# Kernel tuning notes

Hardware: AMD Instinct MI355X
Metric: run time of the kernel (lower is better)

The kernel has to match this reference:

```python
import jax, jax.numpy as jnp
import numpy as np

B, T, C, H = 8, 1024, 1024, 16
D = C // H  # head size 64
EPS = 1e-5

def layernorm(x, g, b):
    m = jnp.mean(x, axis=-1, keepdims=True)
    v = jnp.var(x, axis=-1, keepdims=True)
    return (x - m) * jax.lax.rsqrt(v + EPS) * g + b

def setup_inputs() -> dict:
    key = jax.random.key(0)
    ks = jax.random.split(key, 12)
    s = 1.0 / np.sqrt(C)
    return {
        "x": jax.random.normal(ks[0], (B, T, C), dtype=jnp.float32),
        "mask": jnp.ones((B, 1, 1, T), dtype=jnp.int32),
        "Wq": jax.random.normal(ks[1], (C, C), dtype=jnp.float32) * s,
        "Wk": jax.random.normal(ks[2], (C, C), dtype=jnp.float32) * s,
        "Wv": jax.random.normal(ks[3], (C, C), dtype=jnp.float32) * s,
        "Wo": jax.random.normal(ks[4], (C, C), dtype=jnp.float32) * s,
        "bo": jnp.zeros((C,), dtype=jnp.float32),
        "ln1_g": jnp.ones((C,), dtype=jnp.float32),
        "ln1_b": jnp.zeros((C,), dtype=jnp.float32),
        "ln3_g": jnp.ones((C,), dtype=jnp.float32),
        "ln3_b": jnp.zeros((C,), dtype=jnp.float32),
        "W1": jax.random.normal(ks[5], (C, 4 * C), dtype=jnp.float32) * s,
        "b1": jnp.zeros((4 * C,), dtype=jnp.float32),
        "W2": jax.random.normal(ks[6], (4 * C, C), dtype=jnp.float32) * (1.0 / np.sqrt(4 * C)),
        "b2": jnp.zeros((C,), dtype=jnp.float32),
    }

def reference(x, mask, Wq, Wk, Wv, Wo, bo, ln1_g, ln1_b, ln3_g, ln3_b, W1, b1, W2, b2):
    # --- self-attention sublayer (pre-LN, residual) ---
    xn = layernorm(x, ln1_g, ln1_b)                      # [B,T,C]
    q = (xn @ Wq).reshape(B, T, H, D)                    # [B,T,H,D]
    k = (xn @ Wk).reshape(B, T, H, D)
    v = (xn @ Wv).reshape(B, T, H, D)
    scores = jnp.einsum('bqhd,bkhd->bhqk', q, k) / np.sqrt(D)  # [B,H,T,T]
    scores = jnp.where(mask == 0, -jnp.inf, scores)      # padding mask [B,1,1,T] broadcasts
    attn = jax.nn.softmax(scores, axis=-1)               # dropout=0.0 -> identity
    o = jnp.einsum('bhqk,bkhd->bqhd', attn, v).reshape(B, T, C)
    x = x + o @ Wo + bo
    # --- feed-forward sublayer (pre-LN, residual) ---
    h = layernorm(x, ln3_g, ln3_b)
    ff = jax.nn.relu(h @ W1 + b1) @ W2 + b2
    return x + ff
```

## Files before the change

### kernel.cpp

```cpp
#include <hip/hip_runtime.h>
#include <stdint.h>

typedef unsigned short u16;
typedef __bf16 bf16x8 __attribute__((ext_vector_type(8)));
typedef float f32x4 __attribute__((ext_vector_type(4)));

#define B_ 8
#define T_ 1024
#define C_ 1024
#define H_ 16
#define D_ 64
#define M_TOT 8192
#define FF_ 4096

__device__ __forceinline__ u16 f2bf(float f) {
  union { float f; unsigned u; } c; c.f = f;
  unsigned u = c.u;
  return (u16)((u + 0x7FFFu + ((u >> 16) & 1u)) >> 16);
}

__device__ __forceinline__ void g2l16(const void* g, void* l) {
  __builtin_amdgcn_global_load_lds((const __attribute__((address_space(1))) void*)g,
                                   (__attribute__((address_space(3))) void*)l, 16, 0, 0);
}

__global__ __launch_bounds__(256) void trans_f32_bf16(const float* __restrict__ in,
                                                      u16* __restrict__ out, int R, int C) {
  __shared__ float t[32][33];
  int c0 = blockIdx.x * 32, r0 = blockIdx.y * 32;
  int tx = threadIdx.x & 31, ty = threadIdx.x >> 5;
#pragma unroll
  for (int i = ty; i < 32; i += 8)
    t[i][tx] = in[(size_t)(r0 + i) * C + c0 + tx];
  __syncthreads();
#pragma unroll
  for (int i = ty; i < 32; i += 8)
    out[(size_t)(c0 + i) * R + r0 + tx] = f2bf(t[tx][i]);
}

__global__ __launch_bounds__(256) void ln_f32_bf16(const float* __restrict__ x,
                                                   const float* __restrict__ g,
                                                   const float* __restrict__ bt,
                                                   u16* __restrict__ out) {
  int row = blockIdx.x, tid = threadIdx.x;
  const float4* xr = (const float4*)(x + (size_t)row * C_);
  float4 a = xr[tid];
  float s = a.x + a.y + a.z + a.w;
  float ss = a.x * a.x + a.y * a.y + a.z * a.z + a.w * a.w;
#pragma unroll
  for (int m = 1; m < 64; m <<= 1) { s += __shfl_xor(s, m); ss += __shfl_xor(ss, m); }
  __shared__ float red[8];
  int wave = tid >> 6, lane = tid & 63;
  if (lane == 0) { red[wave] = s; red[wave + 4] = ss; }
  __syncthreads();
  s = red[0] + red[1] + red[2] + red[3];
  ss = red[4] + red[5] + red[6] + red[7];
  float mean = s * (1.0f / C_);
  float rstd = rsqrtf(ss * (1.0f / C_) - mean * mean + 1e-5f);
  float4 gg = ((const float4*)g)[tid];
  float4 bb = ((const float4*)bt)[tid];
  u16* op = out + (size_t)row * C_ + tid * 4;
  op[0] = f2bf((a.x - mean) * rstd * gg.x + bb.x);
  op[1] = f2bf((a.y - mean) * rstd * gg.y + bb.y);
  op[2] = f2bf((a.z - mean) * rstd * gg.z + bb.z);
  op[3] = f2bf((a.w - mean) * rstd * gg.w + bb.w);
}

template <int EPI>
__global__ __launch_bounds__(256) void gemm_bf16(const u16* __restrict__ A,
                                                 const u16* __restrict__ BT,
                                                 u16* __restrict__ outb, float* __restrict__ outf,
                                                 const float* __restrict__ bias,
                                                 const float* __restrict__ resid,
                                                 int M, int N, int K) {
  __shared__ u16 As[128 * 32];
  __shared__ u16 Bs[128 * 32];
  int tid = threadIdx.x, wave = tid >> 6, lane = tid & 63;
  int m0 = blockIdx.y * 128, n0 = blockIdx.x * 128;
  int wr = wave >> 1, wc = wave & 1;
  int frow = lane & 15, fk = (lane >> 4) * 8;
  f32x4 acc[4][4] = {};
  for (int k0 = 0; k0 < K; k0 += 32) {
    __syncthreads();
#pragma unroll
    for (int i = 0; i < 2; i++) {
      int c = i * 256 + tid;
      const u16* ga = A + (size_t)(m0 + (c >> 2)) * K + k0 + (c & 3) * 8;
      const u16* gb = BT + (size_t)(n0 + (c >> 2)) * K + k0 + (c & 3) * 8;
      g2l16(ga, As + (i * 256 + wave * 64) * 8);
      g2l16(gb, Bs + (i * 256 + wave * 64) * 8);
    }
    asm volatile("s_waitcnt vmcnt(0)" ::: "memory");
    __syncthreads();
    bf16x8 af[4], bfr[4];
#pragma unroll
    for (int m = 0; m < 4; m++) af[m] = *(const bf16x8*)(As + (wr * 64 + m * 16 + frow) * 32 + fk);
#pragma unroll
    for (int n = 0; n < 4; n++) bfr[n] = *(const bf16x8*)(Bs + (wc * 64 + n * 16 + frow) * 32 + fk);
#pragma unroll
    for (int m = 0; m < 4; m++)
#pragma unroll
      for (int n = 0; n < 4; n++)
        acc[m][n] = __builtin_amdgcn_mfma_f32_16x16x32_bf16(af[m], bfr[n], acc[m][n], 0, 0, 0);
  }
#pragma unroll
  for (int m = 0; m < 4; m++)
#pragma unroll
    for (int n = 0; n < 4; n++)
#pragma unroll
      for (int r = 0; r < 4; r++) {
        int row = m0 + wr * 64 + m * 16 + (lane >> 4) * 4 + r;
        int col = n0 + wc * 64 + n * 16 + (lane & 15);
        float v = acc[m][n][r];
        if (EPI == 0) {
          outb[(size_t)row * N + col] = f2bf(v);
        } else if (EPI == 1) {
          v += bias[col];
          v = fmaxf(v, 0.f);
          outb[(size_t)row * N + col] = f2bf(v);
        } else {
          v += bias[col] + resid[(size_t)row * N + col];
          outf[(size_t)row * N + col] = v;
        }
      }
}

__global__ __launch_bounds__(256) void attn_kernel(const u16* __restrict__ q,
                                                   const u16* __restrict__ k,
                                                   const u16* __restrict__ v,
                                                   const int* __restrict__ mask,
                                                   u16* __restrict__ o) {
  int tid = threadIdx.x, wave = tid >> 6, lane = tid & 63;
  int qt = blockIdx.x;
  int bh = blockIdx.y;
  int b = bh >> 4, h = bh & 15;
  const size_t base = ((size_t)b * T_) * C_ + h * D_;

  int qrow = qt * 64 + wave * 16 + (lane & 15);
  int dk = (lane >> 4) * 8;
  bf16x8 qf0 = *(const bf16x8*)(q + base + (size_t)qrow * C_ + dk);
  bf16x8 qf1 = *(const bf16x8*)(q + base + (size_t)qrow * C_ + dk + 32);

  f32x4 oacc[4] = {};
  float mrun[4], lrun[4];
#pragma unroll
  for (int r = 0; r < 4; r++) { mrun[r] = -1e30f; lrun[r] = 0.f; }

  __shared__ u16 vlds[32 * 64];
  __shared__ u16 plds[4][16 * 32];

  for (int kt = 0; kt < T_ / 32; ++kt) {
    __syncthreads();
    {
      int c = tid;
      const u16* gv = v + base + (size_t)(kt * 32 + (c >> 3)) * C_ + (c & 7) * 8;
      g2l16(gv, vlds + wave * 512);
    }
    f32x4 s[2];
#pragma unroll
    for (int c = 0; c < 2; c++) {
      int kcol = kt * 32 + c * 16 + (lane & 15);
      const u16* kp = k + base + (size_t)kcol * C_;
      bf16x8 k0 = *(const bf16x8*)(kp + dk);
      bf16x8 k1 = *(const bf16x8*)(kp + dk + 32);
      f32x4 a = {};
      a = __builtin_amdgcn_mfma_f32_16x16x32_bf16(qf0, k0, a, 0, 0, 0);
      a = __builtin_amdgcn_mfma_f32_16x16x32_bf16(qf1, k1, a, 0, 0, 0);
      int mv = mask[b * T_ + kcol];
#pragma unroll
      for (int r = 0; r < 4; r++) {
        float sv = a[r] * 0.125f;
        a[r] = mv ? sv : -1e30f;
      }
      s[c] = a;
    }
    float tmax[4];
#pragma unroll
    for (int r = 0; r < 4; r++) tmax[r] = fmaxf(s[0][r], s[1][r]);
#pragma unroll
    for (int m = 1; m < 16; m <<= 1)
#pragma unroll
      for (int r = 0; r < 4; r++) tmax[r] = fmaxf(tmax[r], __shfl_xor(tmax[r], m));
    float alpha[4];
#pragma unroll
    for (int r = 0; r < 4; r++) {
      float nm = fmaxf(mrun[r], tmax[r]);
      alpha[r] = __expf(mrun[r] - nm);
      mrun[r] = nm;
    }
    float psum[4] = {0.f, 0.f, 0.f, 0.f};
#pragma unroll
    for (int c = 0; c < 2; c++)
#pragma unroll
      for (int r = 0; r < 4; r++) {
        float p = __expf(s[c][r] - mrun[r]);
        s[c][r] = p;
        psum[r] += p;
      }
#pragma unroll
    for (int m = 1; m < 16; m <<= 1)
#pragma unroll
      for (int r = 0; r < 4; r++) psum[r] += __shfl_xor(psum[r], m);
#pragma unroll
    for (int r = 0; r < 4; r++) lrun[r] = lrun[r] * alpha[r] + psum[r];
#pragma unroll
    for (int n = 0; n < 4; n++)
#pragma unroll
      for (int r = 0; r < 4; r++) oacc[n][r] *= alpha[r];
    u16* pw = plds[wave];
#pragma unroll
    for (int c = 0; c < 2; c++)
#pragma unroll
      for (int r = 0; r < 4; r++)
        pw[((lane >> 4) * 4 + r) * 32 + c * 16 + (lane & 15)] = f2bf(s[c][r]);
    bf16x8 pa = *(const bf16x8*)(pw + (lane & 15) * 32 + (lane >> 4) * 8);

    asm volatile("s_waitcnt vmcnt(0)" ::: "memory");
    __syncthreads();
    const __bf16* vp = (const __bf16*)vlds;
#pragma unroll
    for (int n = 0; n < 4; n++) {
      bf16x8 vb;
#pragma unroll
      for (int j = 0; j < 8; j++) vb[j] = vp[((lane >> 4) * 8 + j) * 64 + n * 16 + (lane & 15)];
      oacc[n] = __builtin_amdgcn_mfma_f32_16x16x32_bf16(pa, vb, oacc[n], 0, 0, 0);
    }
  }
#pragma unroll
  for (int n = 0; n < 4; n++)
#pragma unroll
    for (int r = 0; r < 4; r++) {
      int row = qt * 64 + wave * 16 + (lane >> 4) * 4 + r;
      o[((size_t)b * T_ + row) * C_ + h * D_ + n * 16 + (lane & 15)] =
          f2bf(oacc[n][r] / lrun[r]);
    }
}

extern "C" void kernel_launch(void* const* d_in, const int* in_sizes, int n_in,
                              void* d_out, int out_size, void* d_ws, size_t ws_size,
                              hipStream_t stream) {
  const float* x    = (const float*)d_in[0];
  const int*   mask = (const int*)d_in[1];
  const float* Wq   = (const float*)d_in[2];
  const float* Wk   = (const float*)d_in[3];
  const float* Wv   = (const float*)d_in[4];
  const float* Wo   = (const float*)d_in[5];
  const float* bo   = (const float*)d_in[6];
  const float* ln1g = (const float*)d_in[7];
  const float* ln1b = (const float*)d_in[8];
  const float* ln3g = (const float*)d_in[9];
  const float* ln3b = (const float*)d_in[10];
  const float* W1   = (const float*)d_in[11];
  const float* b1   = (const float*)d_in[12];
  const float* W2   = (const float*)d_in[13];
  const float* b2   = (const float*)d_in[14];
  float* out = (float*)d_out;

  char* ws = (char*)d_ws;
  const size_t MB = 1024 * 1024;
  u16* WqT = (u16*)(ws + 0 * MB);
  u16* WkT = (u16*)(ws + 2 * MB);
  u16* WvT = (u16*)(ws + 4 * MB);
  u16* WoT = (u16*)(ws + 6 * MB);
  u16* W1T = (u16*)(ws + 8 * MB);
  u16* W2T = (u16*)(ws + 16 * MB);
  u16* xn  = (u16*)(ws + 24 * MB);
  u16* qb  = (u16*)(ws + 40 * MB);
  u16* kb  = (u16*)(ws + 56 * MB);
  u16* vb  = (u16*)(ws + 72 * MB);
  u16* ob  = (u16*)(ws + 88 * MB);
  float* x2 = (float*)(ws + 104 * MB);
  u16* hb  = xn;
  u16* ff1 = qb;

  dim3 blk(256);
  trans_f32_bf16<<<dim3(32, 32), blk, 0, stream>>>(Wq, WqT, 1024, 1024);
  trans_f32_bf16<<<dim3(32, 32), blk, 0, stream>>>(Wk, WkT, 1024, 1024);
  trans_f32_bf16<<<dim3(32, 32), blk, 0, stream>>>(Wv, WvT, 1024, 1024);
  trans_f32_bf16<<<dim3(32, 32), blk, 0, stream>>>(Wo, WoT, 1024, 1024);
  trans_f32_bf16<<<dim3(128, 32), blk, 0, stream>>>(W1, W1T, 1024, 4096);
  trans_f32_bf16<<<dim3(32, 128), blk, 0, stream>>>(W2, W2T, 4096, 1024);
  ln_f32_bf16<<<8192, blk, 0, stream>>>(x, ln1g, ln1b, xn);
  gemm_bf16<0><<<dim3(8, 64), blk, 0, stream>>>(xn, WqT, qb, nullptr, nullptr, nullptr, 8192, 1024, 1024);
  gemm_bf16<0><<<dim3(8, 64), blk, 0, stream>>>(xn, WkT, kb, nullptr, nullptr, nullptr, 8192, 1024, 1024);
  gemm_bf16<0><<<dim3(8, 64), blk, 0, stream>>>(xn, WvT, vb, nullptr, nullptr, nullptr, 8192, 1024, 1024);
  attn_kernel<<<dim3(16, 128), blk, 0, stream>>>(qb, kb, vb, mask, ob);
  gemm_bf16<2><<<dim3(8, 64), blk, 0, stream>>>(ob, WoT, nullptr, x2, bo, x, 8192, 1024, 1024);
  ln_f32_bf16<<<8192, blk, 0, stream>>>(x2, ln3g, ln3b, hb);
  gemm_bf16<1><<<dim3(32, 64), blk, 0, stream>>>(hb, W1T, ff1, nullptr, b1, nullptr, 8192, 4096, 1024);
  gemm_bf16<2><<<dim3(8, 64), blk, 0, stream>>>(ff1, W2T, nullptr, out, b2, x2, 8192, 1024, 4096);
}
```

Before: 721.1 us.

## Pre-transpose V per head and widen attention key tile to 64 with swizzled P

Adds a kernel that transposes V into a per-(batch,head) [D,T] layout so the attention kernel can load V fragments directly from global memory as contiguous 8-element vectors. This replaces the LDS staging of V, the block-wide barriers and the strided scalar LDS gathers. The key tile grows from 32 to 64 keys per iteration, which halves the number of softmax reductions per key. The P scratch in LDS is padded and XOR-swizzled to reduce bank conflicts. In exchange it adds an extra kernel pass over V and direct global V reads per wave without sharing across waves, relying on cache hits.

```diff
diff --git a/kernel.cpp b/kernel.cpp
--- a/kernel.cpp
+++ b/kernel.cpp
@@ -36,6 +36,22 @@
 #pragma unroll
   for (int i = ty; i < 32; i += 8)
     out[(size_t)(c0 + i) * R + r0 + tx] = f2bf(t[tx][i]);
+}
+
+__global__ __launch_bounds__(256) void vtrans_bf16(const u16* __restrict__ v,
+                                                   u16* __restrict__ vt) {
+  __shared__ u16 t[64][66];
+  int bh = blockIdx.y;
+  int b = bh >> 4, h = bh & 15;
+  int t0 = blockIdx.x * 64;
+  int tx = threadIdx.x & 63, w = threadIdx.x >> 6;
+#pragma unroll
+  for (int i = w; i < 64; i += 4)
+    t[i][tx] = v[(size_t)(b * T_ + t0 + i) * C_ + h * D_ + tx];
+  __syncthreads();
+#pragma unroll
+  for (int d = w; d < 64; d += 4)
+    vt[((size_t)bh * D_ + d) * T_ + t0 + tx] = t[tx][d];
 }
 
 __global__ __launch_bounds__(256) void ln_f32_bf16(const float* __restrict__ x,
@@ -127,7 +143,7 @@
 
 __global__ __launch_bounds__(256) void attn_kernel(const u16* __restrict__ q,
                                                    const u16* __restrict__ k,
-                                                   const u16* __restrict__ v,
+                                                   const u16* __restrict__ vt,
                                                    const int* __restrict__ mask,
                                                    u16* __restrict__ o) {
   int tid = threadIdx.x, wave = tid >> 6, lane = tid & 63;
@@ -135,31 +151,30 @@
   int bh = blockIdx.y;
   int b = bh >> 4, h = bh & 15;
   const size_t base = ((size_t)b * T_) * C_ + h * D_;
-
-  int qrow = qt * 64 + wave * 16 + (lane & 15);
-  int dk = (lane >> 4) * 8;
+  int l15 = lane & 15, g = lane >> 4;
+
+  int qrow = qt * 64 + wave * 16 + l15;
+  int dk = g * 8;
   bf16x8 qf0 = *(const bf16x8*)(q + base + (size_t)qrow * C_ + dk);
   bf16x8 qf1 = *(const bf16x8*)(q + base + (size_t)qrow * C_ + dk + 32);
 
+  const u16* vbase = vt + (size_t)bh * D_ * T_;
+
   f32x4 oacc[4] = {};
   float mrun[4], lrun[4];
 #pragma unroll
   for (int r = 0; r < 4; r++) { mrun[r] = -1e30f; lrun[r] = 0.f; }
 
-  __shared__ u16 vlds[32 * 64];
-  __shared__ u16 plds[4][16 * 32];
-
-  for (int kt = 0; kt < T_ / 32; ++kt) {
-    __syncthreads();
-    {
-      int c = tid;
-      const u16* gv = v + base + (size_t)(kt * 32 + (c >> 3)) * C_ + (c & 7) * 8;
-      g2l16(gv, vlds + wave * 512);
-    }
-    f32x4 s[2];
-#pragma unroll
-    for (int c = 0; c < 2; c++) {
-      int kcol = kt * 32 + c * 16 + (lane & 15);
+  __shared__ u16 plds[4][16 * 72];
+  u16* pw = plds[wave];
+  const int wsw = g * 8;
+  const int rsw = ((l15 >> 2) & 3) * 8;
+
+  for (int kt = 0; kt < T_ / 64; ++kt) {
+    f32x4 s[4];
+#pragma unroll
+    for (int c = 0; c < 4; c++) {
+      int kcol = kt * 64 + c * 16 + l15;
       const u16* kp = k + base + (size_t)kcol * C_;
       bf16x8 k0 = *(const bf16x8*)(kp + dk);
       bf16x8 k1 = *(const bf16x8*)(kp + dk + 32);
@@ -168,15 +183,13 @@
       a = __builtin_amdgcn_mfma_f32_16x16x32_bf16(qf1, k1, a, 0, 0, 0);
       int mv = mask[b * T_ + kcol];
 #pragma unroll
-      for (int r = 0; r < 4; r++) {
-        float sv = a[r] * 0.125f;
-        a[r] = mv ? sv : -1e30f;
-      }
+      for (int r = 0; r < 4; r++) a[r] = mv ? a[r] * 0.125f : -1e30f;
       s[c] = a;
     }
     float tmax[4];
 #pragma unroll
-    for (int r = 0; r < 4; r++) tmax[r] = fmaxf(s[0][r], s[1][r]);
+    for (int r = 0; r < 4; r++)
+      tmax[r] = fmaxf(fmaxf(s[0][r], s[1][r]), fmaxf(s[2][r], s[3][r]));
 #pragma unroll
     for (int m = 1; m < 16; m <<= 1)
 #pragma unroll
@@ -190,7 +203,7 @@
     }
     float psum[4] = {0.f, 0.f, 0.f, 0.f};
 #pragma unroll
-    for (int c = 0; c < 2; c++)
+    for (int c = 0; c < 4; c++)
 #pragma unroll
       for (int r = 0; r < 4; r++) {
         float p = __expf(s[c][r] - mrun[r]);
@@ -207,31 +220,28 @@
     for (int n = 0; n < 4; n++)
 #pragma unroll
       for (int r = 0; r < 4; r++) oacc[n][r] *= alpha[r];
-    u16* pw = plds[wave];
-#pragma unroll
-    for (int c = 0; c < 2; c++)
+#pragma unroll
+    for (int c = 0; c < 4; c++)
 #pragma unroll
       for (int r = 0; r < 4; r++)
-        pw[((lane >> 4) * 4 + r) * 32 + c * 16 + (lane & 15)] = f2bf(s[c][r]);
-    bf16x8 pa = *(const bf16x8*)(pw + (lane & 15) * 32 + (lane >> 4) * 8);
-
-    asm volatile("s_waitcnt vmcnt(0)" ::: "memory");
-    __syncthreads();
-    const __bf16* vp = (const __bf16*)vlds;
+        pw[(4 * g + r) * 72 + ((c * 16 + l15) ^ wsw)] = f2bf(s[c][r]);
+    bf16x8 pa0 = *(const bf16x8*)(pw + l15 * 72 + (0 * 32 + (g * 8 ^ rsw)));
+    bf16x8 pa1 = *(const bf16x8*)(pw + l15 * 72 + (1 * 32 + (g * 8 ^ rsw)));
 #pragma unroll
     for (int n = 0; n < 4; n++) {
-      bf16x8 vb;
-#pragma unroll
-      for (int j = 0; j < 8; j++) vb[j] = vp[((lane >> 4) * 8 + j) * 64 + n * 16 + (lane & 15)];
-      oacc[n] = __builtin_amdgcn_mfma_f32_16x16x32_bf16(pa, vb, oacc[n], 0, 0, 0);
+      const u16* vp = vbase + (size_t)(n * 16 + l15) * T_ + kt * 64 + g * 8;
+      bf16x8 v0 = *(const bf16x8*)(vp);
+      bf16x8 v1 = *(const bf16x8*)(vp + 32);
+      oacc[n] = __builtin_amdgcn_mfma_f32_16x16x32_bf16(pa0, v0, oacc[n], 0, 0, 0);
+      oacc[n] = __builtin_amdgcn_mfma_f32_16x16x32_bf16(pa1, v1, oacc[n], 0, 0, 0);
     }
   }
 #pragma unroll
   for (int n = 0; n < 4; n++)
 #pragma unroll
     for (int r = 0; r < 4; r++) {
-      int row = qt * 64 + wave * 16 + (lane >> 4) * 4 + r;
-      o[((size_t)b * T_ + row) * C_ + h * D_ + n * 16 + (lane & 15)] =
+      int row = qt * 64 + wave * 16 + g * 4 + r;
+      o[((size_t)b * T_ + row) * C_ + h * D_ + n * 16 + l15] =
           f2bf(oacc[n][r] / lrun[r]);
     }
 }
@@ -270,6 +280,7 @@
   u16* vb  = (u16*)(ws + 72 * MB);
   u16* ob  = (u16*)(ws + 88 * MB);
   float* x2 = (float*)(ws + 104 * MB);
+  u16* vT  = xn;
   u16* hb  = xn;
   u16* ff1 = qb;
 
@@ -284,7 +295,8 @@
   gemm_bf16<0><<<dim3(8, 64), blk, 0, stream>>>(xn, WqT, qb, nullptr, nullptr, nullptr, 8192, 1024, 1024);
   gemm_bf16<0><<<dim3(8, 64), blk, 0, stream>>>(xn, WkT, kb, nullptr, nullptr, nullptr, 8192, 1024, 1024);
   gemm_bf16<0><<<dim3(8, 64), blk, 0, stream>>>(xn, WvT, vb, nullptr, nullptr, nullptr, 8192, 1024, 1024);
-  attn_kernel<<<dim3(16, 128), blk, 0, stream>>>(qb, kb, vb, mask, ob);
+  vtrans_bf16<<<dim3(16, 128), blk, 0, stream>>>(vb, vT);
+  attn_kernel<<<dim3(16, 128), blk, 0, stream>>>(qb, kb, vT, mask, ob);
   gemm_bf16<2><<<dim3(8, 64), blk, 0, stream>>>(ob, WoT, nullptr, x2, bo, x, 8192, 1024, 1024);
   ln_f32_bf16<<<8192, blk, 0, stream>>>(x2, ln3g, ln3b, hb);
   gemm_bf16<1><<<dim3(32, 64), blk, 0, stream>>>(hb, W1T, ff1, nullptr, b1, nullptr, 8192, 4096, 1024);
```

New measurement: 749.3 us. 1.04x slower.
